# Optimization experiments

Hardware: AMD Instinct MI355X
Metric: run time of the kernel (lower is better)

Reference implementation:

```python
import jax, jax.numpy as jnp
import numpy as np

MAX_CACHE_LEN = 4096


def _rotate_half(t):
    d = t.shape[-1] // 2
    return jnp.concatenate([-t[..., d:], t[..., :d]], axis=-1)


def _apply_rope(t, cos, sin):
    # t: (B, S, H, D); cos/sin: (S, D)
    c = cos[None, :, None, :]
    s = sin[None, :, None, :]
    return t * c + _rotate_half(t) * s


def setup_inputs() -> dict:
    key = jax.random.key(0)
    ks = jax.random.split(key, 7)
    B, S, E, D, KVH = 1, 2048, 2048, 64, 8
    sc = 0.02
    x = jax.random.normal(ks[0], (B, S, E), dtype=jnp.float32)
    Wq = jax.random.normal(ks[1], (E, E), dtype=jnp.float32) * sc
    Wk = jax.random.normal(ks[2], (KVH * D, E), dtype=jnp.float32) * sc
    Wv = jax.random.normal(ks[3], (KVH * D, E), dtype=jnp.float32) * sc
    Wo = jax.random.normal(ks[4], (E, E), dtype=jnp.float32) * sc
    # RoPE tables
    pos = jnp.arange(S, dtype=jnp.float32)[:, None]
    inv_freq = 1.0 / (10000.0 ** (jnp.arange(0, D, 2, dtype=jnp.float32) / D))
    ang = pos * inv_freq[None, :]              # (S, D/2)
    ang = jnp.concatenate([ang, ang], axis=-1)  # (S, D)
    cos = jnp.cos(ang)
    sin = jnp.sin(ang)
    # additive causal mask (1,1,S,S): 0 where allowed, -1e9 where masked
    causal = jnp.tril(jnp.ones((S, S), dtype=bool))
    attn_mask = jnp.where(causal, 0.0, -1e9).astype(jnp.float32)[None, None]
    return {"x": x, "Wq": Wq, "Wk": Wk, "Wv": Wv, "Wo": Wo,
            "cos": cos, "sin": sin, "attn_mask": attn_mask, "last_pos": S}


def reference(x, Wq, Wk, Wv, Wo, cos, sin, attn_mask, last_pos):
    B, S, E = x.shape
    D = cos.shape[-1]
    H = E // D
    KVH = Wk.shape[0] // D
    group = H // KVH

    q = (x @ Wq.T).reshape(B, S, H, D)
    k = (x @ Wk.T).reshape(B, S, KVH, D)
    v = (x @ Wv.T).reshape(B, S, KVH, D)

    q = _apply_rope(q, cos, sin)
    k = _apply_rope(k, cos, sin)

    # KV-cache write (index_copy at positions [last_pos-S, last_pos)), then slice [:last_pos]
    key_cache = jnp.zeros((B, MAX_CACHE_LEN, KVH, D), dtype=x.dtype)
    value_cache = jnp.zeros((B, MAX_CACHE_LEN, KVH, D), dtype=x.dtype)
    key_cache = jax.lax.dynamic_update_slice(key_cache, jax.lax.stop_gradient(k), (0, last_pos - S, 0, 0))
    value_cache = jax.lax.dynamic_update_slice(value_cache, jax.lax.stop_gradient(v), (0, last_pos - S, 0, 0))
    kc = key_cache[:, :last_pos]    # (B, T, KVH, D)
    vc = value_cache[:, :last_pos]

    # GQA: repeat kv heads to match q heads
    kc = jnp.repeat(kc, group, axis=2)  # (B, T, H, D)
    vc = jnp.repeat(vc, group, axis=2)

    scale = 1.0 / np.sqrt(D)
    scores = jnp.einsum('bqhd,bkhd->bhqk', q, kc) * scale
    scores = scores + attn_mask
    probs = jax.nn.softmax(scores.astype(jnp.float32), axis=-1).astype(x.dtype)
    attn = jnp.einsum('bhqk,bkhd->bqhd', probs, vc)  # (B, S, H, D)
    out = attn.reshape(B, S, E) @ Wo.T
    return out
```

## Files before the change

### kernel.cpp

```cpp
#include <hip/hip_runtime.h>
#include <stdint.h>

typedef unsigned short u16;
typedef unsigned int   u32;

typedef __bf16 bf16x8 __attribute__((ext_vector_type(8)));
typedef float  fx4    __attribute__((ext_vector_type(4)));
typedef u16    u16x8  __attribute__((ext_vector_type(8)));
typedef u16    u16x4  __attribute__((ext_vector_type(4)));

typedef __attribute__((address_space(1))) unsigned int as1_u32;
typedef __attribute__((address_space(3))) unsigned int as3_u32;

__device__ __forceinline__ void gload_lds16(const void* g, void* lds) {
  __builtin_amdgcn_global_load_lds((const as1_u32*)(uintptr_t)g,
                                   (as3_u32*)(uintptr_t)lds, 16, 0, 0);
}

__device__ __forceinline__ float b2f(u32 bits) {
  union { u32 i; float f; } v; v.i = bits << 16; return v.f;
}
__device__ __forceinline__ u16 f2b(float f) {
  union { float f; u32 i; } v; v.f = f;
  u32 x = v.i;
  return (u16)((x + 0x7fffu + ((x >> 16) & 1u)) >> 16);
}
__device__ __forceinline__ u16 f2b_hw(float f) {
  union { __bf16 b; u16 u; } v; v.b = (__bf16)f; return v.u;
}

__global__ __launch_bounds__(256) void cast_kernel(
    const float* __restrict__ s0, const float* __restrict__ s1,
    const float* __restrict__ s2, const float* __restrict__ s3,
    const float* __restrict__ s4, u16* __restrict__ dst)
{
  const size_t i8 = ((size_t)blockIdx.x * 256 + threadIdx.x) * 8;
  if (i8 >= 14680064) return;
  const float* src; size_t off;
  if      (i8 <  4194304) { src = s0; off = i8; }
  else if (i8 <  8388608) { src = s1; off = i8 - 4194304; }
  else if (i8 <  9437184) { src = s2; off = i8 - 8388608; }
  else if (i8 < 10485760) { src = s3; off = i8 - 9437184; }
  else                    { src = s4; off = i8 - 10485760; }
  const float4 a = *(const float4*)(src + off);
  const float4 b = *(const float4*)(src + off + 4);
  u16x8 o;
  o[0] = f2b(a.x); o[1] = f2b(a.y); o[2] = f2b(a.z); o[3] = f2b(a.w);
  o[4] = f2b(b.x); o[5] = f2b(b.y); o[6] = f2b(b.z); o[7] = f2b(b.w);
  *(u16x8*)(dst + i8) = o;
}

template <int MODE>
__global__ __launch_bounds__(256) void gemm_bt(
    const u16* __restrict__ A, const u16* __restrict__ B0,
    const u16* __restrict__ B1, const u16* __restrict__ B2,
    void* __restrict__ Cv, int K, int split1, int split2, int ldc,
    const float* __restrict__ cosb, const float* __restrict__ sinb,
    u16* __restrict__ vtg)
{
  __shared__ __align__(16) u16 smem[4 * 8192];

  const int n0 = blockIdx.x * 128;
  const int m0 = blockIdx.y * 128;

  const u16* Bsel; int nb;
  if (n0 < split1)      { Bsel = B0; nb = n0; }
  else if (n0 < split2) { Bsel = B1; nb = n0 - split1; }
  else                  { Bsel = B2; nb = n0 - split2; }

  const int tid  = threadIdx.x;
  const int wave = tid >> 6, lane = tid & 63;
  const int wm = wave >> 1, wn = wave & 1;
  const int quad = lane >> 4, l16 = lane & 15;

  fx4 acc[4][4];
#pragma unroll
  for (int i = 0; i < 4; ++i)
#pragma unroll
    for (int j = 0; j < 4; ++j) acc[i][j] = fx4{0.f, 0.f, 0.f, 0.f};

  const int row = tid >> 2;
  const int cc  = (tid & 3) * 8;
  auto stage = [&](int kt) {
    u16* As = smem + (kt & 3) * 8192;
    u16* Bs = As + 4096;
    const int k0 = kt * 32;
#pragma unroll
    for (int i = 0; i < 2; ++i) {
      const int r2 = row + i * 64;
      const int s  = tid + i * 256;
      gload_lds16(A    + (size_t)(m0 + r2) * K + k0 + cc, As + s * 8);
      gload_lds16(Bsel + (size_t)(nb + r2) * K + k0 + cc, Bs + s * 8);
    }
  };

  const int KT = K >> 5;
  stage(0); stage(1); stage(2);

#pragma unroll 1
  for (int kt = 0; kt < KT; ++kt) {
    const int rem = KT - 1 - kt;
    if (rem >= 3)      asm volatile("s_waitcnt vmcnt(12)\n\ts_barrier" ::: "memory");
    else if (rem == 2) asm volatile("s_waitcnt vmcnt(8)\n\ts_barrier" ::: "memory");
    else if (rem == 1) asm volatile("s_waitcnt vmcnt(4)\n\ts_barrier" ::: "memory");
    else               asm volatile("s_waitcnt vmcnt(0)\n\ts_barrier" ::: "memory");
    if (kt + 3 < KT) stage(kt + 3);

    const u16* As = smem + (kt & 3) * 8192;
    const u16* Bs = As + 4096;

    bf16x8 af[4], bfr[4];
#pragma unroll
    for (int t = 0; t < 4; ++t) {
      af[t]  = *(const bf16x8*)&As[(wm * 64 + t * 16 + l16) * 32 + quad * 8];
      bfr[t] = *(const bf16x8*)&Bs[(wn * 64 + t * 16 + l16) * 32 + quad * 8];
    }
#pragma unroll
    for (int ti = 0; ti < 4; ++ti)
#pragma unroll
      for (int tj = 0; tj < 4; ++tj)
        acc[ti][tj] = __builtin_amdgcn_mfma_f32_16x16x32_bf16(
            af[ti], bfr[tj], acc[ti][tj], 0, 0, 0);
  }

  if (MODE == 1) {
    float* C = (float*)Cv;
#pragma unroll
    for (int ti = 0; ti < 4; ++ti) {
      const int row_b = m0 + wm * 64 + ti * 16 + quad * 4;
#pragma unroll
      for (int tj = 0; tj < 4; ++tj) {
        const int col = n0 + wn * 64 + tj * 16 + l16;
#pragma unroll
        for (int r = 0; r < 4; ++r)
          C[(size_t)(row_b + r) * ldc + col] = acc[ti][tj][r];
      }
    }
  } else {
    u16* C = (u16*)Cv;
    const int cb = n0 + wn * 64;
    if (cb < 2560) {
      const float qs = (cb < 2048) ? 0.125f : 1.0f;
#pragma unroll
      for (int ti = 0; ti < 4; ++ti) {
#pragma unroll
        for (int r = 0; r < 4; ++r) {
          const int s = m0 + wm * 64 + ti * 16 + quad * 4 + r;
          const float* cr = cosb + s * 64;
          const float* sr = sinb + s * 64;
          u16* orow = C + (size_t)s * 3072 + cb;
#pragma unroll
          for (int tj = 0; tj < 2; ++tj) {
            const int d0 = tj * 16 + l16, d1 = d0 + 32;
            const float x0 = acc[ti][tj][r], x1 = acc[ti][tj + 2][r];
            orow[d0] = f2b((x0 * cr[d0] - x1 * sr[d0]) * qs);
            orow[d1] = f2b((x1 * cr[d1] + x0 * sr[d1]) * qs);
          }
        }
      }
    } else {
      const int vr0 = cb - 2560;
#pragma unroll
      for (int ti = 0; ti < 4; ++ti) {
        const int s0 = m0 + wm * 64 + ti * 16 + quad * 4;
#pragma unroll
        for (int tj = 0; tj < 4; ++tj) {
          const int vr = vr0 + tj * 16 + l16;
          u16x4 o;
#pragma unroll
          for (int r = 0; r < 4; ++r) o[r] = f2b(acc[ti][tj][r]);
          *(u16x4*)(vtg + (size_t)vr * 2048 + s0) = o;
        }
      }
    }
  }
}

__global__ __launch_bounds__(256) void attn_kernel(
    const u16* __restrict__ qkv, const u16* __restrict__ vt,
    u16* __restrict__ attnbuf)
{
  const int h   = blockIdx.y;
  const int kvh = h >> 2;
  const int tid = threadIdx.x;
  const int w = tid >> 6, lane = tid & 63;
  const int quad = lane >> 4, l16 = lane & 15;

  __shared__ __align__(16) u16 Qs[64][72];
  __shared__ __align__(16) u16 Ks[128][72];
  __shared__ __align__(16) u16 Vh[2][64][72];
  __shared__ __align__(16) u16 Ps[4][16][72];

  const int kcol = 2048 + kvh * 64;

#pragma unroll 1
  for (int pass = 0; pass < 2; ++pass) {
    const int bx = pass ? (31 - blockIdx.x) : blockIdx.x;
    const int r0 = bx * 64;
    const int nhalf  = bx + 1;
    const int ntiles = (bx + 2) >> 1;

    __syncthreads();

#pragma unroll
    for (int i = 0; i < 2; ++i) {
      const int idx = tid + i * 256;
      const int r = idx >> 3, dc = (idx & 7) * 8;
      *(uint4*)&Qs[r][dc] =
          *(const uint4*)(qkv + (size_t)(r0 + r) * 3072 + h * 64 + dc);
    }

    fx4 O[4];
    float l_r[4];
#pragma unroll
    for (int c = 0; c < 4; ++c) O[c] = fx4{0.f, 0.f, 0.f, 0.f};
#pragma unroll
    for (int r = 0; r < 4; ++r) l_r[r] = 0.f;

#pragma unroll 1
    for (int kt = 0; kt < ntiles; ++kt) {
      const int k0 = kt * 128;
      __syncthreads();
#pragma unroll
      for (int i = 0; i < 4; ++i) {
        const int idx = tid + i * 256;
        const int j = idx >> 3, dc = (idx & 7) * 8;
        *(uint4*)&Ks[j][dc] =
            *(const uint4*)(qkv + (size_t)(k0 + j) * 3072 + kcol + dc);
      }
#pragma unroll
      for (int i = 0; i < 4; ++i) {
        const int idx = tid + i * 256;
        const int hh = idx >> 9, rem = idx & 511;
        const int j = rem >> 3, dc = (rem & 7) * 8;
        *(uint4*)&Vh[hh][j][dc] =
            *(const uint4*)(vt + (size_t)(kvh * 64 + j) * 2048 + k0 + hh * 64 + dc);
      }
      __syncthreads();

      const bf16x8 aq0 = *(const bf16x8*)&Qs[w * 16 + l16][quad * 8];
      const bf16x8 aq1 = *(const bf16x8*)&Qs[w * 16 + l16][32 + quad * 8];

#pragma unroll
      for (int hh = 0; hh < 2; ++hh) {
        const int half = kt * 2 + hh;
        if (half < nhalf) {
          const int k0h = k0 + hh * 64;

          fx4 sc[4];
#pragma unroll
          for (int c = 0; c < 4; ++c) {
            const bf16x8 b0 = *(const bf16x8*)&Ks[hh * 64 + c * 16 + l16][quad * 8];
            const bf16x8 b1 = *(const bf16x8*)&Ks[hh * 64 + c * 16 + l16][32 + quad * 8];
            fx4 z = fx4{0.f, 0.f, 0.f, 0.f};
            z     = __builtin_amdgcn_mfma_f32_16x16x32_bf16(aq0, b0, z, 0, 0, 0);
            sc[c] = __builtin_amdgcn_mfma_f32_16x16x32_bf16(aq1, b1, z, 0, 0, 0);
          }

          if (k0h >= r0) {
#pragma unroll
            for (int c = 0; c < 4; ++c)
#pragma unroll
              for (int r = 0; r < 4; ++r) {
                float p = __expf(sc[c][r]);
                if (k0h + c * 16 + l16 > r0 + w * 16 + quad * 4 + r) p = 0.f;
                l_r[r] += p;
                Ps[w][quad * 4 + r][c * 16 + l16] = f2b_hw(p);
              }
          } else {
#pragma unroll
            for (int c = 0; c < 4; ++c)
#pragma unroll
              for (int r = 0; r < 4; ++r) {
                const float p = __expf(sc[c][r]);
                l_r[r] += p;
                Ps[w][quad * 4 + r][c * 16 + l16] = f2b_hw(p);
              }
          }

          const bf16x8 ap0 = *(const bf16x8*)&Ps[w][l16][quad * 8];
          const bf16x8 ap1 = *(const bf16x8*)&Ps[w][l16][32 + quad * 8];
#pragma unroll
          for (int c = 0; c < 4; ++c) {
            const bf16x8 v0 = *(const bf16x8*)&Vh[hh][c * 16 + l16][quad * 8];
            const bf16x8 v1 = *(const bf16x8*)&Vh[hh][c * 16 + l16][32 + quad * 8];
            O[c] = __builtin_amdgcn_mfma_f32_16x16x32_bf16(ap0, v0, O[c], 0, 0, 0);
            O[c] = __builtin_amdgcn_mfma_f32_16x16x32_bf16(ap1, v1, O[c], 0, 0, 0);
          }
        }
      }
    }

#pragma unroll
    for (int r = 0; r < 4; ++r) {
      float l = l_r[r];
#pragma unroll
      for (int off = 1; off < 16; off <<= 1) l += __shfl_xor(l, off, 64);
      const float inv = 1.f / fmaxf(l, 1e-30f);
      const int qg = r0 + w * 16 + quad * 4 + r;
#pragma unroll
      for (int c = 0; c < 4; ++c)
        attnbuf[(size_t)qg * 2048 + h * 64 + c * 16 + l16] = f2b(O[c][r] * inv);
    }
  }
}

extern "C" void kernel_launch(void* const* d_in, const int* in_sizes, int n_in,
                              void* d_out, int out_size, void* d_ws, size_t ws_size,
                              hipStream_t stream) {
  const float* x    = (const float*)d_in[0];
  const float* Wq   = (const float*)d_in[1];
  const float* Wk   = (const float*)d_in[2];
  const float* Wv   = (const float*)d_in[3];
  const float* Wo   = (const float*)d_in[4];
  const float* cosb = (const float*)d_in[5];
  const float* sinb = (const float*)d_in[6];
  float* out = (float*)d_out;

  u16* ws      = (u16*)d_ws;
  u16* qkv     = ws;
  u16* attnbuf = ws + 6291456;
  u16* xb      = ws + 10485760;
  u16* Wqb     = ws + 14680064;
  u16* Wkb     = ws + 18874368;
  u16* Wvb     = ws + 19922944;
  u16* Wob     = ws + 20971520;
  u16* vtg     = ws + 25165824;

  cast_kernel<<<7168, 256, 0, stream>>>(x, Wq, Wk, Wv, Wo, xb);

  gemm_bt<0><<<dim3(24, 16), 256, 0, stream>>>(
      xb, Wqb, Wkb, Wvb, qkv, 2048, 2048, 2560, 3072, cosb, sinb, vtg);

  attn_kernel<<<dim3(16, 32), 256, 0, stream>>>(qkv, vtg, attnbuf);

  gemm_bt<1><<<dim3(16, 16), 256, 0, stream>>>(
      attnbuf, Wob, Wob, Wob, out, 2048, 1 << 30, 1 << 30, 2048, cosb, sinb, vtg);
}
```

Before: 229.8 us.

## Pre-pack operands into MFMA fragment order and load GEMM tiles directly to registers

The cast kernel now writes x and the weights in a packed layout that matches the MFMA fragment order, and the attention kernel writes its output in the same packed layout. The GEMMs drop LDS staging and barriers: each wave loads its fragments straight from global memory with register double-buffering. This removes LDS traffic and synchronisation, but waves no longer share tiles through LDS, so global/L2 reads double and the deeper async prefetch pipeline is lost.

```diff
diff --git a/kernel.cpp b/kernel.cpp
--- a/kernel.cpp
+++ b/kernel.cpp
@@ -9,14 +9,6 @@
 typedef u16    u16x8  __attribute__((ext_vector_type(8)));
 typedef u16    u16x4  __attribute__((ext_vector_type(4)));
 
-typedef __attribute__((address_space(1))) unsigned int as1_u32;
-typedef __attribute__((address_space(3))) unsigned int as3_u32;
-
-__device__ __forceinline__ void gload_lds16(const void* g, void* lds) {
-  __builtin_amdgcn_global_load_lds((const as1_u32*)(uintptr_t)g,
-                                   (as3_u32*)(uintptr_t)lds, 16, 0, 0);
-}
-
 __device__ __forceinline__ float b2f(u32 bits) {
   union { u32 i; float f; } v; v.i = bits << 16; return v.f;
 }
@@ -29,99 +21,102 @@
   union { __bf16 b; u16 u; } v; v.b = (__bf16)f; return v.u;
 }
 
-__global__ __launch_bounds__(256) void cast_kernel(
+
+__global__ __launch_bounds__(256) void cast_pack_kernel(
     const float* __restrict__ s0, const float* __restrict__ s1,
     const float* __restrict__ s2, const float* __restrict__ s3,
-    const float* __restrict__ s4, u16* __restrict__ dst)
+    const float* __restrict__ s4, u16* __restrict__ xp,
+    u16* __restrict__ wqkvp, u16* __restrict__ wop)
 {
   const size_t i8 = ((size_t)blockIdx.x * 256 + threadIdx.x) * 8;
   if (i8 >= 14680064) return;
-  const float* src; size_t off;
-  if      (i8 <  4194304) { src = s0; off = i8; }
-  else if (i8 <  8388608) { src = s1; off = i8 - 4194304; }
-  else if (i8 <  9437184) { src = s2; off = i8 - 8388608; }
-  else if (i8 < 10485760) { src = s3; off = i8 - 9437184; }
-  else                    { src = s4; off = i8 - 10485760; }
+  const float* src; size_t off; u16* dst; int nbase;
+  if      (i8 <  4194304) { src = s0; off = i8;            dst = xp;    nbase = 0; }
+  else if (i8 <  8388608) { src = s1; off = i8 - 4194304;  dst = wqkvp; nbase = 0; }
+  else if (i8 <  9437184) { src = s2; off = i8 - 8388608;  dst = wqkvp; nbase = 2048; }
+  else if (i8 < 10485760) { src = s3; off = i8 - 9437184;  dst = wqkvp; nbase = 2560; }
+  else                    { src = s4; off = i8 - 10485760; dst = wop;   nbase = 0; }
+
   const float4 a = *(const float4*)(src + off);
   const float4 b = *(const float4*)(src + off + 4);
   u16x8 o;
   o[0] = f2b(a.x); o[1] = f2b(a.y); o[2] = f2b(a.z); o[3] = f2b(a.w);
   o[4] = f2b(b.x); o[5] = f2b(b.y); o[6] = f2b(b.z); o[7] = f2b(b.w);
-  *(u16x8*)(dst + i8) = o;
+
+  const int n  = nbase + (int)(off >> 11);
+  const int k  = (int)(off & 2047);
+  const int n64 = n >> 6, t = (n >> 4) & 3;
+  const int kt = k >> 5, quad = (k >> 3) & 3;
+  const int lane = quad * 16 + (n & 15);
+  const size_t dest = ((((size_t)n64 * 64 + kt) * 4 + t) * 64 + lane) * 8;
+  *(u16x8*)(dst + dest) = o;
 }
 
 template <int MODE>
-__global__ __launch_bounds__(256) void gemm_bt(
-    const u16* __restrict__ A, const u16* __restrict__ B0,
-    const u16* __restrict__ B1, const u16* __restrict__ B2,
-    void* __restrict__ Cv, int K, int split1, int split2, int ldc,
+__global__ __launch_bounds__(256) void gemm_flat(
+    const u16* __restrict__ Ap, const u16* __restrict__ Bp,
+    void* __restrict__ Cv, int ldc,
     const float* __restrict__ cosb, const float* __restrict__ sinb,
     u16* __restrict__ vtg)
 {
-  __shared__ __align__(16) u16 smem[4 * 8192];
-
-  const int n0 = blockIdx.x * 128;
-  const int m0 = blockIdx.y * 128;
-
-  const u16* Bsel; int nb;
-  if (n0 < split1)      { Bsel = B0; nb = n0; }
-  else if (n0 < split2) { Bsel = B1; nb = n0 - split1; }
-  else                  { Bsel = B2; nb = n0 - split2; }
-
   const int tid  = threadIdx.x;
   const int wave = tid >> 6, lane = tid & 63;
   const int wm = wave >> 1, wn = wave & 1;
   const int quad = lane >> 4, l16 = lane & 15;
 
+  const int m64 = blockIdx.y * 2 + wm;
+  const int n64 = blockIdx.x * 2 + wn;
+
+  const u16* ap = Ap + (size_t)m64 * 131072 + lane * 8;
+  const u16* bp = Bp + (size_t)n64 * 131072 + lane * 8;
+
   fx4 acc[4][4];
 #pragma unroll
   for (int i = 0; i < 4; ++i)
 #pragma unroll
     for (int j = 0; j < 4; ++j) acc[i][j] = fx4{0.f, 0.f, 0.f, 0.f};
 
-  const int row = tid >> 2;
-  const int cc  = (tid & 3) * 8;
-  auto stage = [&](int kt) {
-    u16* As = smem + (kt & 3) * 8192;
-    u16* Bs = As + 4096;
-    const int k0 = kt * 32;
-#pragma unroll
-    for (int i = 0; i < 2; ++i) {
-      const int r2 = row + i * 64;
-      const int s  = tid + i * 256;
-      gload_lds16(A    + (size_t)(m0 + r2) * K + k0 + cc, As + s * 8);
-      gload_lds16(Bsel + (size_t)(nb + r2) * K + k0 + cc, Bs + s * 8);
-    }
-  };
-
-  const int KT = K >> 5;
-  stage(0); stage(1); stage(2);
+  bf16x8 a0[4], b0[4], a1[4], b1[4];
+#pragma unroll
+  for (int t = 0; t < 4; ++t) {
+    a0[t] = *(const bf16x8*)(ap + t * 512);
+    b0[t] = *(const bf16x8*)(bp + t * 512);
+  }
 
 #pragma unroll 1
-  for (int kt = 0; kt < KT; ++kt) {
-    const int rem = KT - 1 - kt;
-    if (rem >= 3)      asm volatile("s_waitcnt vmcnt(12)\n\ts_barrier" ::: "memory");
-    else if (rem == 2) asm volatile("s_waitcnt vmcnt(8)\n\ts_barrier" ::: "memory");
-    else if (rem == 1) asm volatile("s_waitcnt vmcnt(4)\n\ts_barrier" ::: "memory");
-    else               asm volatile("s_waitcnt vmcnt(0)\n\ts_barrier" ::: "memory");
-    if (kt + 3 < KT) stage(kt + 3);
-
-    const u16* As = smem + (kt & 3) * 8192;
-    const u16* Bs = As + 4096;
-
-    bf16x8 af[4], bfr[4];
+  for (int kt = 0; kt < 64; kt += 2) {
+    const u16* ap1 = ap + (size_t)(kt + 1) * 2048;
+    const u16* bp1 = bp + (size_t)(kt + 1) * 2048;
 #pragma unroll
     for (int t = 0; t < 4; ++t) {
-      af[t]  = *(const bf16x8*)&As[(wm * 64 + t * 16 + l16) * 32 + quad * 8];
-      bfr[t] = *(const bf16x8*)&Bs[(wn * 64 + t * 16 + l16) * 32 + quad * 8];
+      a1[t] = *(const bf16x8*)(ap1 + t * 512);
+      b1[t] = *(const bf16x8*)(bp1 + t * 512);
     }
 #pragma unroll
     for (int ti = 0; ti < 4; ++ti)
 #pragma unroll
       for (int tj = 0; tj < 4; ++tj)
         acc[ti][tj] = __builtin_amdgcn_mfma_f32_16x16x32_bf16(
-            af[ti], bfr[tj], acc[ti][tj], 0, 0, 0);
+            a0[ti], b0[tj], acc[ti][tj], 0, 0, 0);
+    if (kt < 62) {
+      const u16* ap2 = ap + (size_t)(kt + 2) * 2048;
+      const u16* bp2 = bp + (size_t)(kt + 2) * 2048;
+#pragma unroll
+      for (int t = 0; t < 4; ++t) {
+        a0[t] = *(const bf16x8*)(ap2 + t * 512);
+        b0[t] = *(const bf16x8*)(bp2 + t * 512);
+      }
+    }
+#pragma unroll
+    for (int ti = 0; ti < 4; ++ti)
+#pragma unroll
+      for (int tj = 0; tj < 4; ++tj)
+        acc[ti][tj] = __builtin_amdgcn_mfma_f32_16x16x32_bf16(
+            a1[ti], b1[tj], acc[ti][tj], 0, 0, 0);
   }
+
+  const int m0 = blockIdx.y * 128;
+  const int n0 = blockIdx.x * 128;
 
   if (MODE == 1) {
     float* C = (float*)Cv;
@@ -298,9 +293,14 @@
       for (int off = 1; off < 16; off <<= 1) l += __shfl_xor(l, off, 64);
       const float inv = 1.f / fmaxf(l, 1e-30f);
       const int qg = r0 + w * 16 + quad * 4 + r;
-#pragma unroll
-      for (int c = 0; c < 4; ++c)
-        attnbuf[(size_t)qg * 2048 + h * 64 + c * 16 + l16] = f2b(O[c][r] * inv);
+      const int m64 = qg >> 6, t = (qg >> 4) & 3, ql = qg & 15;
+#pragma unroll
+      for (int c = 0; c < 4; ++c) {
+        const int col = h * 64 + c * 16 + l16;
+        const int kt = col >> 5, qd = (col >> 3) & 3, j = col & 7;
+        attnbuf[((((size_t)m64 * 64 + kt) * 4 + t) * 64 + qd * 16 + ql) * 8 + j] =
+            f2b(O[c][r] * inv);
+      }
     }
   }
 }
@@ -320,20 +320,18 @@
   u16* ws      = (u16*)d_ws;
   u16* qkv     = ws;
   u16* attnbuf = ws + 6291456;
-  u16* xb      = ws + 10485760;
-  u16* Wqb     = ws + 14680064;
-  u16* Wkb     = ws + 18874368;
-  u16* Wvb     = ws + 19922944;
-  u16* Wob     = ws + 20971520;
+  u16* xp      = ws + 10485760;
+  u16* wqkvp   = ws + 14680064;
+  u16* wop     = ws + 20971520;
   u16* vtg     = ws + 25165824;
 
-  cast_kernel<<<7168, 256, 0, stream>>>(x, Wq, Wk, Wv, Wo, xb);
-
-  gemm_bt<0><<<dim3(24, 16), 256, 0, stream>>>(
-      xb, Wqb, Wkb, Wvb, qkv, 2048, 2048, 2560, 3072, cosb, sinb, vtg);
+  cast_pack_kernel<<<7168, 256, 0, stream>>>(x, Wq, Wk, Wv, Wo, xp, wqkvp, wop);
+
+  gemm_flat<0><<<dim3(24, 16), 256, 0, stream>>>(
+      xp, wqkvp, qkv, 3072, cosb, sinb, vtg);
 
   attn_kernel<<<dim3(16, 32), 256, 0, stream>>>(qkv, vtg, attnbuf);
 
-  gemm_bt<1><<<dim3(16, 16), 256, 0, stream>>>(
-      attnbuf, Wob, Wob, Wob, out, 2048, 1 << 30, 1 << 30, 2048, cosb, sinb, vtg);
-}
+  gemm_flat<1><<<dim3(16, 16), 256, 0, stream>>>(
+      attnbuf, wop, out, 2048, cosb, sinb, vtg);
+}
```

Result: slower. 262.1 us (+14.1%).

## Give each wave private double-buffered LDS tiles to remove block barriers in GEMM

Applied to the files above, without the earlier changes.

The GEMM stops sharing a 128x32 A/B tile across the four waves. Each wave now loads its own 64-row A and 64-row B slices into private LDS, double-buffered, and waits only on its own vmcnt, with no s_barrier. This removes block-wide synchronisation. In exchange, global/L2 traffic per block doubles because A and B rows are loaded redundantly by two waves each, and the prefetch depth drops from three stages to one.

```diff
diff --git a/kernel.cpp b/kernel.cpp
--- a/kernel.cpp
+++ b/kernel.cpp
@@ -51,14 +51,14 @@
 }
 
 template <int MODE>
-__global__ __launch_bounds__(256) void gemm_bt(
+__global__ __launch_bounds__(256) void gemm_wp(
     const u16* __restrict__ A, const u16* __restrict__ B0,
     const u16* __restrict__ B1, const u16* __restrict__ B2,
     void* __restrict__ Cv, int K, int split1, int split2, int ldc,
     const float* __restrict__ cosb, const float* __restrict__ sinb,
     u16* __restrict__ vtg)
 {
-  __shared__ __align__(16) u16 smem[4 * 8192];
+  __shared__ __align__(16) u16 smem[4][2][4096];
 
   const int n0 = blockIdx.x * 128;
   const int m0 = blockIdx.y * 128;
@@ -73,47 +73,50 @@
   const int wm = wave >> 1, wn = wave & 1;
   const int quad = lane >> 4, l16 = lane & 15;
 
+  const int am = m0 + wm * 64;
+  const int bn = nb + wn * 64;
+
+  const int srow = lane >> 2;
+  const int scol = (lane & 3) * 8;
+
+  auto stage = [&](int kt, int b) {
+    const int k0 = kt * 32;
+    u16* dA = &smem[wave][b][0];
+    u16* dB = &smem[wave][b][2048];
+#pragma unroll
+    for (int i = 0; i < 4; ++i) {
+      gload_lds16(A    + (size_t)(am + i * 16 + srow) * K + k0 + scol,
+                  dA + i * 512 + lane * 8);
+      gload_lds16(Bsel + (size_t)(bn + i * 16 + srow) * K + k0 + scol,
+                  dB + i * 512 + lane * 8);
+    }
+  };
+
   fx4 acc[4][4];
 #pragma unroll
   for (int i = 0; i < 4; ++i)
 #pragma unroll
     for (int j = 0; j < 4; ++j) acc[i][j] = fx4{0.f, 0.f, 0.f, 0.f};
 
-  const int row = tid >> 2;
-  const int cc  = (tid & 3) * 8;
-  auto stage = [&](int kt) {
-    u16* As = smem + (kt & 3) * 8192;
-    u16* Bs = As + 4096;
-    const int k0 = kt * 32;
-#pragma unroll
-    for (int i = 0; i < 2; ++i) {
-      const int r2 = row + i * 64;
-      const int s  = tid + i * 256;
-      gload_lds16(A    + (size_t)(m0 + r2) * K + k0 + cc, As + s * 8);
-      gload_lds16(Bsel + (size_t)(nb + r2) * K + k0 + cc, Bs + s * 8);
-    }
-  };
-
   const int KT = K >> 5;
-  stage(0); stage(1); stage(2);
+  stage(0, 0);
 
 #pragma unroll 1
   for (int kt = 0; kt < KT; ++kt) {
-    const int rem = KT - 1 - kt;
-    if (rem >= 3)      asm volatile("s_waitcnt vmcnt(12)\n\ts_barrier" ::: "memory");
-    else if (rem == 2) asm volatile("s_waitcnt vmcnt(8)\n\ts_barrier" ::: "memory");
-    else if (rem == 1) asm volatile("s_waitcnt vmcnt(4)\n\ts_barrier" ::: "memory");
-    else               asm volatile("s_waitcnt vmcnt(0)\n\ts_barrier" ::: "memory");
-    if (kt + 3 < KT) stage(kt + 3);
-
-    const u16* As = smem + (kt & 3) * 8192;
-    const u16* Bs = As + 4096;
-
+    if (kt + 1 < KT) {
+      stage(kt + 1, (kt + 1) & 1);
+      asm volatile("s_waitcnt vmcnt(8)" ::: "memory");
+    } else {
+      asm volatile("s_waitcnt vmcnt(0)" ::: "memory");
+    }
+
+    const u16* Asw = &smem[wave][kt & 1][0];
+    const u16* Bsw = &smem[wave][kt & 1][2048];
     bf16x8 af[4], bfr[4];
 #pragma unroll
     for (int t = 0; t < 4; ++t) {
-      af[t]  = *(const bf16x8*)&As[(wm * 64 + t * 16 + l16) * 32 + quad * 8];
-      bfr[t] = *(const bf16x8*)&Bs[(wn * 64 + t * 16 + l16) * 32 + quad * 8];
+      af[t]  = *(const bf16x8*)&Asw[(t * 16 + l16) * 32 + quad * 8];
+      bfr[t] = *(const bf16x8*)&Bsw[(t * 16 + l16) * 32 + quad * 8];
     }
 #pragma unroll
     for (int ti = 0; ti < 4; ++ti)
@@ -329,11 +332,11 @@
 
   cast_kernel<<<7168, 256, 0, stream>>>(x, Wq, Wk, Wv, Wo, xb);
 
-  gemm_bt<0><<<dim3(24, 16), 256, 0, stream>>>(
+  gemm_wp<0><<<dim3(24, 16), 256, 0, stream>>>(
       xb, Wqb, Wkb, Wvb, qkv, 2048, 2048, 2560, 3072, cosb, sinb, vtg);
 
   attn_kernel<<<dim3(16, 32), 256, 0, stream>>>(qkv, vtg, attnbuf);
 
-  gemm_bt<1><<<dim3(16, 16), 256, 0, stream>>>(
+  gemm_wp<1><<<dim3(16, 16), 256, 0, stream>>>(
       attnbuf, Wob, Wob, Wob, out, 2048, 1 << 30, 1 << 30, 2048, cosb, sinb, vtg);
 }
```

Result: slower. 243.6 us (+6.0%).

## Use 2 waves per attention block with 32 query rows each to reuse K/V fragments

Applied to the files above, without the earlier changes.

Halves the attention block to 128 threads, so each wave owns 32 query rows (two 16-row MFMA tiles) instead of 16. Each K and V fragment read from LDS now feeds two MFMAs, which cuts LDS read traffic per MFMA. The Q fragments are hoisted out of the key-tile loop, and the final store uses the hardware bf16 convert. In exchange each wave holds more registers, fewer waves are resident to hide global-load latency, and each thread issues twice as many K/V tile loads.

```diff
diff --git a/kernel.cpp b/kernel.cpp
--- a/kernel.cpp
+++ b/kernel.cpp
@@ -176,7 +176,7 @@
   }
 }
 
-__global__ __launch_bounds__(256) void attn_kernel(
+__global__ __launch_bounds__(128) void attn_kernel(
     const u16* __restrict__ qkv, const u16* __restrict__ vt,
     u16* __restrict__ attnbuf)
 {
@@ -189,7 +189,7 @@
   __shared__ __align__(16) u16 Qs[64][72];
   __shared__ __align__(16) u16 Ks[128][72];
   __shared__ __align__(16) u16 Vh[2][64][72];
-  __shared__ __align__(16) u16 Ps[4][16][72];
+  __shared__ __align__(16) u16 Ps[2][32][72];
 
   const int kcol = 2048 + kvh * 64;
 
@@ -203,34 +203,46 @@
     __syncthreads();
 
 #pragma unroll
-    for (int i = 0; i < 2; ++i) {
-      const int idx = tid + i * 256;
+    for (int i = 0; i < 4; ++i) {
+      const int idx = tid + i * 128;
       const int r = idx >> 3, dc = (idx & 7) * 8;
       *(uint4*)&Qs[r][dc] =
           *(const uint4*)(qkv + (size_t)(r0 + r) * 3072 + h * 64 + dc);
     }
-
-    fx4 O[4];
-    float l_r[4];
-#pragma unroll
-    for (int c = 0; c < 4; ++c) O[c] = fx4{0.f, 0.f, 0.f, 0.f};
-#pragma unroll
-    for (int r = 0; r < 4; ++r) l_r[r] = 0.f;
+    __syncthreads();
+
+    bf16x8 aq[2][2];
+#pragma unroll
+    for (int t = 0; t < 2; ++t) {
+      aq[t][0] = *(const bf16x8*)&Qs[w * 32 + t * 16 + l16][quad * 8];
+      aq[t][1] = *(const bf16x8*)&Qs[w * 32 + t * 16 + l16][32 + quad * 8];
+    }
+
+    fx4 O[2][4];
+    float l_r[2][4];
+#pragma unroll
+    for (int t = 0; t < 2; ++t)
+#pragma unroll
+      for (int c = 0; c < 4; ++c) O[t][c] = fx4{0.f, 0.f, 0.f, 0.f};
+#pragma unroll
+    for (int t = 0; t < 2; ++t)
+#pragma unroll
+      for (int r = 0; r < 4; ++r) l_r[t][r] = 0.f;
 
 #pragma unroll 1
     for (int kt = 0; kt < ntiles; ++kt) {
       const int k0 = kt * 128;
       __syncthreads();
 #pragma unroll
-      for (int i = 0; i < 4; ++i) {
-        const int idx = tid + i * 256;
+      for (int i = 0; i < 8; ++i) {
+        const int idx = tid + i * 128;
         const int j = idx >> 3, dc = (idx & 7) * 8;
         *(uint4*)&Ks[j][dc] =
             *(const uint4*)(qkv + (size_t)(k0 + j) * 3072 + kcol + dc);
       }
 #pragma unroll
-      for (int i = 0; i < 4; ++i) {
-        const int idx = tid + i * 256;
+      for (int i = 0; i < 8; ++i) {
+        const int idx = tid + i * 128;
         const int hh = idx >> 9, rem = idx & 511;
         const int j = rem >> 3, dc = (rem & 7) * 8;
         *(uint4*)&Vh[hh][j][dc] =
@@ -238,70 +250,84 @@
       }
       __syncthreads();
 
-      const bf16x8 aq0 = *(const bf16x8*)&Qs[w * 16 + l16][quad * 8];
-      const bf16x8 aq1 = *(const bf16x8*)&Qs[w * 16 + l16][32 + quad * 8];
-
 #pragma unroll
       for (int hh = 0; hh < 2; ++hh) {
         const int half = kt * 2 + hh;
         if (half < nhalf) {
           const int k0h = k0 + hh * 64;
 
-          fx4 sc[4];
+          fx4 sc[2][4];
 #pragma unroll
           for (int c = 0; c < 4; ++c) {
             const bf16x8 b0 = *(const bf16x8*)&Ks[hh * 64 + c * 16 + l16][quad * 8];
             const bf16x8 b1 = *(const bf16x8*)&Ks[hh * 64 + c * 16 + l16][32 + quad * 8];
-            fx4 z = fx4{0.f, 0.f, 0.f, 0.f};
-            z     = __builtin_amdgcn_mfma_f32_16x16x32_bf16(aq0, b0, z, 0, 0, 0);
-            sc[c] = __builtin_amdgcn_mfma_f32_16x16x32_bf16(aq1, b1, z, 0, 0, 0);
+#pragma unroll
+            for (int t = 0; t < 2; ++t) {
+              fx4 z = fx4{0.f, 0.f, 0.f, 0.f};
+              z        = __builtin_amdgcn_mfma_f32_16x16x32_bf16(aq[t][0], b0, z, 0, 0, 0);
+              sc[t][c] = __builtin_amdgcn_mfma_f32_16x16x32_bf16(aq[t][1], b1, z, 0, 0, 0);
+            }
           }
 
           if (k0h >= r0) {
 #pragma unroll
-            for (int c = 0; c < 4; ++c)
-#pragma unroll
-              for (int r = 0; r < 4; ++r) {
-                float p = __expf(sc[c][r]);
-                if (k0h + c * 16 + l16 > r0 + w * 16 + quad * 4 + r) p = 0.f;
-                l_r[r] += p;
-                Ps[w][quad * 4 + r][c * 16 + l16] = f2b_hw(p);
-              }
+            for (int t = 0; t < 2; ++t)
+#pragma unroll
+              for (int c = 0; c < 4; ++c)
+#pragma unroll
+                for (int r = 0; r < 4; ++r) {
+                  float p = __expf(sc[t][c][r]);
+                  if (k0h + c * 16 + l16 > r0 + w * 32 + t * 16 + quad * 4 + r) p = 0.f;
+                  l_r[t][r] += p;
+                  Ps[w][t * 16 + quad * 4 + r][c * 16 + l16] = f2b_hw(p);
+                }
           } else {
 #pragma unroll
-            for (int c = 0; c < 4; ++c)
-#pragma unroll
-              for (int r = 0; r < 4; ++r) {
-                const float p = __expf(sc[c][r]);
-                l_r[r] += p;
-                Ps[w][quad * 4 + r][c * 16 + l16] = f2b_hw(p);
-              }
-          }
-
-          const bf16x8 ap0 = *(const bf16x8*)&Ps[w][l16][quad * 8];
-          const bf16x8 ap1 = *(const bf16x8*)&Ps[w][l16][32 + quad * 8];
+            for (int t = 0; t < 2; ++t)
+#pragma unroll
+              for (int c = 0; c < 4; ++c)
+#pragma unroll
+                for (int r = 0; r < 4; ++r) {
+                  const float p = __expf(sc[t][c][r]);
+                  l_r[t][r] += p;
+                  Ps[w][t * 16 + quad * 4 + r][c * 16 + l16] = f2b_hw(p);
+                }
+          }
+
+          bf16x8 ap[2][2];
+#pragma unroll
+          for (int t = 0; t < 2; ++t) {
+            ap[t][0] = *(const bf16x8*)&Ps[w][t * 16 + l16][quad * 8];
+            ap[t][1] = *(const bf16x8*)&Ps[w][t * 16 + l16][32 + quad * 8];
+          }
 #pragma unroll
           for (int c = 0; c < 4; ++c) {
             const bf16x8 v0 = *(const bf16x8*)&Vh[hh][c * 16 + l16][quad * 8];
             const bf16x8 v1 = *(const bf16x8*)&Vh[hh][c * 16 + l16][32 + quad * 8];
-            O[c] = __builtin_amdgcn_mfma_f32_16x16x32_bf16(ap0, v0, O[c], 0, 0, 0);
-            O[c] = __builtin_amdgcn_mfma_f32_16x16x32_bf16(ap1, v1, O[c], 0, 0, 0);
+#pragma unroll
+            for (int t = 0; t < 2; ++t) {
+              O[t][c] = __builtin_amdgcn_mfma_f32_16x16x32_bf16(ap[t][0], v0, O[t][c], 0, 0, 0);
+              O[t][c] = __builtin_amdgcn_mfma_f32_16x16x32_bf16(ap[t][1], v1, O[t][c], 0, 0, 0);
+            }
           }
         }
       }
     }
 
 #pragma unroll
-    for (int r = 0; r < 4; ++r) {
-      float l = l_r[r];
-#pragma unroll
-      for (int off = 1; off < 16; off <<= 1) l += __shfl_xor(l, off, 64);
-      const float inv = 1.f / fmaxf(l, 1e-30f);
-      const int qg = r0 + w * 16 + quad * 4 + r;
-#pragma unroll
-      for (int c = 0; c < 4; ++c)
-        attnbuf[(size_t)qg * 2048 + h * 64 + c * 16 + l16] = f2b(O[c][r] * inv);
-    }
+    for (int t = 0; t < 2; ++t)
+#pragma unroll
+      for (int r = 0; r < 4; ++r) {
+        float l = l_r[t][r];
+#pragma unroll
+        for (int off = 1; off < 16; off <<= 1) l += __shfl_xor(l, off, 64);
+        const float inv = 1.f / fmaxf(l, 1e-30f);
+        const int qg = r0 + w * 32 + t * 16 + quad * 4 + r;
+#pragma unroll
+        for (int c = 0; c < 4; ++c)
+          attnbuf[(size_t)qg * 2048 + h * 64 + c * 16 + l16] =
+              f2b_hw(O[t][c][r] * inv);
+      }
   }
 }
 
@@ -332,7 +358,7 @@
   gemm_bt<0><<<dim3(24, 16), 256, 0, stream>>>(
       xb, Wqb, Wkb, Wvb, qkv, 2048, 2048, 2560, 3072, cosb, sinb, vtg);
 
-  attn_kernel<<<dim3(16, 32), 256, 0, stream>>>(qkv, vtg, attnbuf);
+  attn_kernel<<<dim3(16, 32), 128, 0, stream>>>(qkv, vtg, attnbuf);
 
   gemm_bt<1><<<dim3(16, 16), 256, 0, stream>>>(
       attnbuf, Wob, Wob, Wob, out, 2048, 1 << 30, 1 << 30, 2048, cosb, sinb, vtg);
```

After: 235.0 us. +2.3%, slower.
